# Kernel tuning notes

Measured on AMD Instinct MI355X. Metric: run time of the kernel, lower is better.

Reference implementation:

```python
import jax, jax.numpy as jnp
import numpy as np

H = 16  # num_heads

def _split_heads(x, h):
    B, T, D = x.shape
    return x.reshape(B, T, h, D // h).transpose(0, 2, 1, 3)  # [B,h,T,d]

def setup_inputs() -> dict:
    key = jax.random.key(0)
    ks = jax.random.split(key, 7)
    B, T, D = 2, 2048, 2048
    s = 0.02
    return {
        "x": jax.random.normal(ks[0], (B, T, D), dtype=jnp.float32),
        "Wq1": jax.random.normal(ks[1], (D, D), dtype=jnp.float32) * s,
        "Wq2": jax.random.normal(ks[2], (D, D), dtype=jnp.float32) * s,
        "Wk": jax.random.normal(ks[3], (D, D), dtype=jnp.float32) * s,
        "Wv": jax.random.normal(ks[4], (D, D), dtype=jnp.float32) * s,
        "Wlam": jax.random.normal(ks[5], (D, H), dtype=jnp.float32) * s,
        "Wo": jax.random.normal(ks[6], (D, D), dtype=jnp.float32) * s,
    }

def reference(x, Wq1, Wq2, Wk, Wv, Wlam, Wo):
    B, T, D = x.shape
    d = D // H
    q1 = _split_heads(x @ Wq1, H)
    q2 = _split_heads(x @ Wq2, H)
    k = _split_heads(x @ Wk, H)
    v = _split_heads(x @ Wv, H)
    q = jnp.concatenate([q1, q2], axis=1)        # [B,2H,T,d] (q1 heads then q2 heads)
    k2 = jnp.repeat(k, 2, axis=1)                # [B,2H,T,d] (adjacent duplication, as torch repeat_interleave)
    v2 = jnp.repeat(v, 2, axis=1)
    scale = 1.0 / jnp.sqrt(jnp.asarray(d, dtype=x.dtype))
    scores = jnp.einsum("bhqd,bhkd->bhqk", q, k2) * scale
    causal = jnp.tril(jnp.ones((T, T), dtype=bool))
    scores = jnp.where(causal, scores, jnp.finfo(scores.dtype).min)
    p = jax.nn.softmax(scores, axis=-1)
    y = jnp.einsum("bhqk,bhkd->bhqd", p, v2)     # [B,2H,T,d]
    y1, y2 = y[:, :H], y[:, H:]
    lam = jax.nn.sigmoid(x @ Wlam).transpose(0, 2, 1)[..., None]  # [B,H,T,1]
    y = y1 - lam * y2                            # [B,H,T,d]
    y = y.transpose(0, 2, 1, 3).reshape(B, T, D)
    return y @ Wo
```

## Files before the change

kernel.cpp:

```cpp
#include <hip/hip_runtime.h>
#include <stdint.h>

#define Bb 2
#define Tt 2048
#define Dd 2048
#define Hh 16
#define HD 128
#define NTOK (Bb*Tt)

typedef _Float16 f16;
typedef unsigned short u16;
typedef __attribute__((ext_vector_type(8))) _Float16 f16x8;
typedef __attribute__((ext_vector_type(4))) _Float16 f16x4;
typedef __attribute__((ext_vector_type(4))) float f32x4;

__device__ __forceinline__ void gl2lds16(const f16* g, f16* l) {
  __builtin_amdgcn_global_load_lds(
      (const __attribute__((address_space(1))) unsigned int*)(const_cast<f16*>(g)),
      (__attribute__((address_space(3))) unsigned int*)(l),
      16, 0, 0);
}

__global__ __launch_bounds__(256) void cvtlam_kernel(const float* __restrict__ x,
                                                     const float* __restrict__ Wlam,
                                                     f16* __restrict__ xh,
                                                     float* __restrict__ lamb) {
  const int wid = threadIdx.x >> 6, lane = threadIdx.x & 63;
  const int tok = blockIdx.x * 4 + wid;
  const float* xr = x + (size_t)tok * Dd;
  f16* xo = xh + (size_t)tok * Dd;
  float acc[16] = {};
#pragma unroll
  for (int j = 0; j < 8; ++j) {
    const int k0 = j * 256 + lane * 4;
    float4 v = *(const float4*)(xr + k0);
    f16x4 o;
    o.x = (f16)v.x; o.y = (f16)v.y; o.z = (f16)v.z; o.w = (f16)v.w;
    *(f16x4*)(xo + k0) = o;
    const float xe4[4] = {v.x, v.y, v.z, v.w};
#pragma unroll
    for (int e = 0; e < 4; ++e) {
      const float xe = xe4[e];
      const float4* wr = (const float4*)(Wlam + (size_t)(k0 + e) * Hh);
#pragma unroll
      for (int q = 0; q < 4; ++q) {
        float4 w = wr[q];
        acc[q * 4 + 0] = fmaf(xe, w.x, acc[q * 4 + 0]);
        acc[q * 4 + 1] = fmaf(xe, w.y, acc[q * 4 + 1]);
        acc[q * 4 + 2] = fmaf(xe, w.z, acc[q * 4 + 2]);
        acc[q * 4 + 3] = fmaf(xe, w.w, acc[q * 4 + 3]);
      }
    }
  }
#pragma unroll
  for (int ofs = 32; ofs >= 1; ofs >>= 1)
#pragma unroll
    for (int i = 0; i < 16; ++i) acc[i] += __shfl_xor(acc[i], ofs);
  if (lane == 0) {
#pragma unroll
    for (int i = 0; i < 16; ++i)
      lamb[tok * Hh + i] = 1.f / (1.f + __expf(-acc[i]));
  }
}

__global__ void wtrans_kernel(const float* __restrict__ W0, const float* __restrict__ W1,
                              const float* __restrict__ W2, const float* __restrict__ W3,
                              const float* __restrict__ W4, f16* __restrict__ wt) {
  const float* W;
  int z = blockIdx.z;
  if (z == 0) W = W0; else if (z == 1) W = W1; else if (z == 2) W = W2;
  else if (z == 3) W = W3; else W = W4;
  f16* dst = wt + (size_t)z * Dd * Dd;
  __shared__ f16 tile[64][65];
  const int k0 = blockIdx.y * 64, n0 = blockIdx.x * 64;
  const int tr = threadIdx.x >> 6, tc = threadIdx.x & 63;
#pragma unroll
  for (int p = 0; p < 16; ++p) {
    int r = tr + p * 4;
    tile[r][tc] = (f16)W[(size_t)(k0 + r) * Dd + n0 + tc];
  }
  __syncthreads();
#pragma unroll
  for (int p = 0; p < 16; ++p) {
    int r = tr + p * 4;
    dst[(size_t)(n0 + r) * Dd + k0 + tc] = tile[tc][r];
  }
}

template <int OUTF16>
__global__ __launch_bounds__(256) void gemm_bt_kernel(
    const f16* __restrict__ A, const f16* __restrict__ Bt0,
    unsigned long long bt_stride, void* __restrict__ Cb, unsigned long long c_stride) {
  __shared__ __align__(16) f16 Alds[128 * 32];
  __shared__ __align__(16) f16 Blds[128 * 32];
  const f16* Bt = Bt0 + (size_t)blockIdx.z * bt_stride;
  const int m0 = blockIdx.y * 128, n0 = blockIdx.x * 128;
  const int tid = threadIdx.x, wid = tid >> 6, lane = tid & 63;
  const int quad = lane >> 4, l15 = lane & 15;
  const int srow = lane >> 2, sch = lane & 3;
  const int g = (l15 >> 1) & 3;
  const int koff = (quad ^ g) * 8;
  const int mw = (wid >> 1) * 64, nw = (wid & 1) * 64;
  const int sg = sch ^ ((srow >> 1) & 3);
  f32x4 acc[4][4] = {};
  for (int kk = 0; kk < Dd; kk += 32) {
#pragma unroll
    for (int j = 0; j < 2; ++j) {
      const int c = wid * 2 + j;
      const int row = c * 16 + srow;
      gl2lds16(A + (size_t)(m0 + row) * Dd + kk + sg * 8, &Alds[c * 512]);
      gl2lds16(Bt + (size_t)(n0 + row) * Dd + kk + sg * 8, &Blds[c * 512]);
    }
    __syncthreads();
    f16x8 af[4], bfr[4];
#pragma unroll
    for (int t = 0; t < 4; ++t)
      af[t] = *(const f16x8*)&Alds[(mw + t * 16 + l15) * 32 + koff];
#pragma unroll
    for (int t = 0; t < 4; ++t)
      bfr[t] = *(const f16x8*)&Blds[(nw + t * 16 + l15) * 32 + koff];
#pragma unroll
    for (int mt = 0; mt < 4; ++mt)
#pragma unroll
      for (int nt = 0; nt < 4; ++nt)
        acc[mt][nt] = __builtin_amdgcn_mfma_f32_16x16x32_f16(af[mt], bfr[nt], acc[mt][nt], 0, 0, 0);
    __syncthreads();
  }
  const size_t czoff = (size_t)blockIdx.z * c_stride;
#pragma unroll
  for (int mt = 0; mt < 4; ++mt) {
    const int r0 = m0 + mw + mt * 16 + quad * 4;
#pragma unroll
    for (int r = 0; r < 4; ++r) {
#pragma unroll
      for (int nt = 0; nt < 4; ++nt) {
        const int col = n0 + nw + nt * 16 + l15;
        const float v = acc[mt][nt][r];
        if (OUTF16)
          ((f16*)Cb)[czoff + (size_t)(r0 + r) * Dd + col] = (f16)v;
        else
          ((float*)Cb)[czoff + (size_t)(r0 + r) * Dd + col] = v;
      }
    }
  }
}

__global__ void vtrans_kernel(const f16* __restrict__ vb, f16* __restrict__ vtb) {
  const int z = blockIdx.z;
  const int b = z >> 4, hv = z & 15;
  const int t0 = blockIdx.x * 64, d0 = blockIdx.y * 64;
  __shared__ f16 tile[64][65];
  const int tr = threadIdx.x >> 6, tc = threadIdx.x & 63;
#pragma unroll
  for (int p = 0; p < 16; ++p) {
    int r = tr + p * 4;
    tile[r][tc] = vb[(size_t)(b * Tt + t0 + r) * Dd + hv * HD + d0 + tc];
  }
  __syncthreads();
  const int u = tc & 31;
  const int tp = (tc & 32) | (((u >> 2) & 3) * 8 + ((u >> 4) & 1) * 4 + (u & 3));
#pragma unroll
  for (int p = 0; p < 16; ++p) {
    int r = tr + p * 4;
    vtb[((size_t)z * HD + d0 + r) * Tt + t0 + tp] = tile[tc][r];
  }
}

__global__ __launch_bounds__(256, 3) void attn_kernel(
    const f16* __restrict__ q1b, const f16* __restrict__ q2b,
    const f16* __restrict__ kbuf, const f16* __restrict__ vtb,
    f16* __restrict__ yah) {
  __shared__ __align__(16) f16 Klds[64 * 128];
  __shared__ __align__(16) f16 Vlds[2][128 * 64];
  const int bx = blockIdx.x;
  const int qt = (bx & 1) ? (15 - (bx >> 1)) : (bx >> 1);
  const int h = blockIdx.y, b = blockIdx.z;
  const int hkv = h >> 1;
  const f16* qb = (h < Hh) ? q1b : q2b;
  const int hq = h & 15;
  const int tid = threadIdx.x, wid = tid >> 6, lane = tid & 63;
  const int quad = lane >> 4, l15 = lane & 15;
  const int qbase = qt * 128 + wid * 32;
  const int ntiles = 2 * qt + 2;
  const f16 qscale = (f16)(0.08838834764831845f * 1.4426950408889634f);

  f16x8 qf0[4], qf1[4];
  {
    const f16* qp0 = qb + (size_t)(b * Tt + qbase + l15) * Dd + hq * HD + quad * 8;
    const f16* qp1 = qp0 + (size_t)16 * Dd;
#pragma unroll
    for (int ks = 0; ks < 4; ++ks) { qf0[ks] = *(const f16x8*)(qp0 + ks * 32); qf1[ks] = *(const f16x8*)(qp1 + ks * 32); }
#pragma unroll
    for (int ks = 0; ks < 4; ++ks) { qf0[ks] *= qscale; qf1[ks] *= qscale; }
  }

  uint32_t koffg[4], voffg[4];
#pragma unroll
  for (int p = 0; p < 4; ++p) {
    const int krow = wid * 16 + p * 4 + (lane >> 4);
    const int kch = (lane & 15) ^ (krow & 7);
    koffg[p] = (uint32_t)((b * Tt + krow) * Dd + hkv * HD + kch * 8);
    const int vrow = wid * 32 + p * 8 + (lane >> 3);
    const int vch = (lane & 7) ^ (vrow & 7);
    voffg[p] = (uint32_t)(((b * 16 + hkv) * HD + vrow) * Tt + vch * 8);
  }

  f32x4 o0[8] = {}, o1[8] = {};
  float m_0 = -3.0e38f, m_1 = -3.0e38f, l_0 = 0.f, l_1 = 0.f;

#define ISSUE_K(KT)                                                                \
  {                                                                                \
    const uint32_t kshift = (uint32_t)(KT) * 64 * Dd;                              \
    _Pragma("unroll") for (int p = 0; p < 4; ++p)                                  \
        gl2lds16(kbuf + kshift + koffg[p], &Klds[(wid * 16 + p * 4) * 128]);       \
  }
#define ISSUE_V(KT)                                                                \
  {                                                                                \
    const uint32_t vshift = (uint32_t)(KT) * 64;                                   \
    f16* vb_ = &Vlds[(KT) & 1][0];                                                 \
    _Pragma("unroll") for (int p = 0; p < 4; ++p)                                  \
        gl2lds16(vtb + vshift + voffg[p], &vb_[(wid * 32 + p * 8) * 64]);          \
  }

  ISSUE_K(0);
  ISSUE_V(0);

  for (int kt = 0; kt < ntiles; ++kt) {
    asm volatile("s_waitcnt vmcnt(4)\n\ts_barrier" ::: "memory");
    const bool live = (kt * 64 <= qbase + 31);
    f32x4 s0[4] = {}, s1[4] = {};
    if (live) {
#pragma unroll
      for (int nt = 0; nt < 4; ++nt) {
        const int r = nt * 16 + l15;
#pragma unroll
        for (int ks = 0; ks < 4; ++ks) {
          f16x8 kf = *(const f16x8*)&Klds[r * 128 + (((ks * 4 + quad) ^ (l15 & 7)) << 3)];
          s0[nt] = __builtin_amdgcn_mfma_f32_16x16x32_f16(kf, qf0[ks], s0[nt], 0, 0, 0);
          s1[nt] = __builtin_amdgcn_mfma_f32_16x16x32_f16(kf, qf1[ks], s1[nt], 0, 0, 0);
        }
      }
    }
    asm volatile("s_waitcnt vmcnt(0) lgkmcnt(0)\n\ts_barrier" ::: "memory");
    if (kt + 1 < ntiles) { ISSUE_K(kt + 1); ISSUE_V(kt + 1); }
    if (live) {
      const f16* Vl = &Vlds[kt & 1][0];
      if (kt * 64 + 63 > qbase) {
        const int q0 = qbase + l15, q1_ = q0 + 16;
#pragma unroll
        for (int nt = 0; nt < 4; ++nt) {
          const int keyb = kt * 64 + nt * 16 + quad * 4;
#pragma unroll
          for (int r = 0; r < 4; ++r) {
            if (keyb + r > q0) s0[nt][r] = -3.0e38f;
            if (keyb + r > q1_) s1[nt][r] = -3.0e38f;
          }
        }
      }
      float tm0 = s0[0][0], tm1 = s1[0][0];
#pragma unroll
      for (int nt = 0; nt < 4; ++nt)
#pragma unroll
        for (int r = 0; r < 4; ++r) { tm0 = fmaxf(tm0, s0[nt][r]); tm1 = fmaxf(tm1, s1[nt][r]); }
      tm0 = fmaxf(tm0, __shfl_xor(tm0, 16)); tm1 = fmaxf(tm1, __shfl_xor(tm1, 16));
      tm0 = fmaxf(tm0, __shfl_xor(tm0, 32)); tm1 = fmaxf(tm1, __shfl_xor(tm1, 32));
      const float mo0 = m_0, mo1 = m_1;
      m_0 = fmaxf(m_0, tm0); m_1 = fmaxf(m_1, tm1);
      float rs0 = 0.f, rs1 = 0.f;
      f16x4 pf0[4], pf1[4];
#pragma unroll
      for (int nt = 0; nt < 4; ++nt) {
        float a0 = exp2f(s0[nt][0] - m_0), a1 = exp2f(s0[nt][1] - m_0);
        float a2 = exp2f(s0[nt][2] - m_0), a3 = exp2f(s0[nt][3] - m_0);
        float b0 = exp2f(s1[nt][0] - m_1), b1 = exp2f(s1[nt][1] - m_1);
        float b2 = exp2f(s1[nt][2] - m_1), b3 = exp2f(s1[nt][3] - m_1);
        rs0 += (a0 + a1) + (a2 + a3);
        rs1 += (b0 + b1) + (b2 + b3);
        pf0[nt].x = (f16)a0; pf0[nt].y = (f16)a1; pf0[nt].z = (f16)a2; pf0[nt].w = (f16)a3;
        pf1[nt].x = (f16)b0; pf1[nt].y = (f16)b1; pf1[nt].z = (f16)b2; pf1[nt].w = (f16)b3;
      }
      rs0 += __shfl_xor(rs0, 16); rs1 += __shfl_xor(rs1, 16);
      rs0 += __shfl_xor(rs0, 32); rs1 += __shfl_xor(rs1, 32);
      if (__ballot((m_0 > mo0) | (m_1 > mo1))) {
        const float al0 = exp2f(mo0 - m_0), al1 = exp2f(mo1 - m_1);
        l_0 *= al0; l_1 *= al1;
        float ar0[4], ar1[4];
#pragma unroll
        for (int r = 0; r < 4; ++r) { ar0[r] = __shfl(al0, quad * 4 + r); ar1[r] = __shfl(al1, quad * 4 + r); }
#pragma unroll
        for (int n2 = 0; n2 < 8; ++n2)
#pragma unroll
          for (int r = 0; r < 4; ++r) { o0[n2][r] *= ar0[r]; o1[n2][r] *= ar1[r]; }
      }
      l_0 += rs0; l_1 += rs1;
#pragma unroll
      for (int g = 0; g < 2; ++g) {
#pragma unroll
        for (int n2 = 0; n2 < 8; ++n2) {
          const int d_ = n2 * 16 + l15;
          f16x8 vf = *(const f16x8*)&Vl[d_ * 64 + (((g * 4 + quad) ^ (l15 & 7)) << 3)];
          f16x4 vlo = __builtin_shufflevector(vf, vf, 0, 1, 2, 3);
          f16x4 vhi = __builtin_shufflevector(vf, vf, 4, 5, 6, 7);
          o0[n2] = __builtin_amdgcn_mfma_f32_16x16x16f16(pf0[2 * g], vlo, o0[n2], 0, 0, 0);
          o0[n2] = __builtin_amdgcn_mfma_f32_16x16x16f16(pf0[2 * g + 1], vhi, o0[n2], 0, 0, 0);
          o1[n2] = __builtin_amdgcn_mfma_f32_16x16x16f16(pf1[2 * g], vlo, o1[n2], 0, 0, 0);
          o1[n2] = __builtin_amdgcn_mfma_f32_16x16x16f16(pf1[2 * g + 1], vhi, o1[n2], 0, 0, 0);
        }
      }
    }
  }
#undef ISSUE_K
#undef ISSUE_V

  float lr0[4], lr1[4];
#pragma unroll
  for (int r = 0; r < 4; ++r) { lr0[r] = __shfl(l_0, quad * 4 + r); lr1[r] = __shfl(l_1, quad * 4 + r); }
#pragma unroll
  for (int r = 0; r < 4; ++r) {
    const float i0 = 1.0f / lr0[r], i1 = 1.0f / lr1[r];
    const int row0 = qbase + quad * 4 + r;
    f16* d0_ = yah + ((size_t)(b * 32 + h) * Tt + row0) * HD;
    f16* d1_ = d0_ + (size_t)16 * HD;
#pragma unroll
    for (int n2 = 0; n2 < 8; ++n2) {
      d0_[n2 * 16 + l15] = (f16)(o0[n2][r] * i0);
      d1_[n2 * 16 + l15] = (f16)(o1[n2][r] * i1);
    }
  }
}

__global__ void combine_kernel(const f16* __restrict__ yah, const float* __restrict__ lamb,
                               f16* __restrict__ ybf) {
  const int n4 = NTOK * Dd / 4;
  int i = blockIdx.x * 256 + threadIdx.x;
  const int stride = gridDim.x * 256;
  for (; i < n4; i += stride) {
    const int e0 = i * 4;
    const int dc = e0 & 127;
    const int hh = (e0 >> 7) & 15;
    const int tt = (e0 >> 11) & 2047;
    const int bb = e0 >> 22;
    const size_t base1 = ((size_t)(bb * 32 + hh) * Tt + tt) * HD + dc;
    const size_t base2 = ((size_t)(bb * 32 + 16 + hh) * Tt + tt) * HD + dc;
    f16x4 y1 = *(const f16x4*)(yah + base1);
    f16x4 y2 = *(const f16x4*)(yah + base2);
    const float lam = lamb[(bb * Tt + tt) * Hh + hh];
    f16x4 o;
    o.x = (f16)((float)y1.x - lam * (float)y2.x);
    o.y = (f16)((float)y1.y - lam * (float)y2.y);
    o.z = (f16)((float)y1.z - lam * (float)y2.z);
    o.w = (f16)((float)y1.w - lam * (float)y2.w);
    *(f16x4*)(ybf + e0) = o;
  }
}

extern "C" void kernel_launch(void* const* d_in, const int* in_sizes, int n_in,
                              void* d_out, int out_size, void* d_ws, size_t ws_size,
                              hipStream_t stream) {
  const float* x    = (const float*)d_in[0];
  const float* Wq1  = (const float*)d_in[1];
  const float* Wq2  = (const float*)d_in[2];
  const float* Wk   = (const float*)d_in[3];
  const float* Wv   = (const float*)d_in[4];
  const float* Wlam = (const float*)d_in[5];
  const float* Wo   = (const float*)d_in[6];

  f16* xbf = (f16*)d_ws;
  f16* wt  = xbf + (size_t)NTOK * Dd;
  f16* q1b = wt + 5ull * Dd * Dd;
  f16* q2b = q1b + (size_t)NTOK * Dd;
  f16* kbf = q2b + (size_t)NTOK * Dd;
  f16* vbf = kbf + (size_t)NTOK * Dd;
  f16* vtb = vbf + (size_t)NTOK * Dd;
  float* lamb = (float*)(vtb + (size_t)NTOK * Dd);
  f16* yah = (f16*)(lamb + (size_t)NTOK * Hh);
  f16* ybf = xbf;

  cvtlam_kernel<<<dim3(NTOK / 4), dim3(256), 0, stream>>>(x, Wlam, xbf, lamb);
  wtrans_kernel<<<dim3(32, 32, 5), dim3(256), 0, stream>>>(Wq1, Wq2, Wk, Wv, Wo, wt);
  gemm_bt_kernel<1><<<dim3(16, 32, 4), dim3(256), 0, stream>>>(
      xbf, wt, (unsigned long long)Dd * Dd, (void*)q1b, (unsigned long long)NTOK * Dd);
  vtrans_kernel<<<dim3(32, 2, 32), dim3(256), 0, stream>>>(vbf, vtb);
  attn_kernel<<<dim3(16, 32, 2), dim3(256), 0, stream>>>(q1b, q2b, kbf, vtb, yah);
  combine_kernel<<<dim3(2048), dim3(256), 0, stream>>>(yah, lamb, ybf);
  gemm_bt_kernel<0><<<dim3(16, 32, 1), dim3(256), 0, stream>>>(
      ybf, wt + 4ull * Dd * Dd, 0ull, d_out, 0ull);
}
```

Measured before the change: 774.9 us.

## Enlarge attention blocks to 8 waves with double-buffered K/V tiles

```diff
diff --git a/kernel.cpp b/kernel.cpp
--- a/kernel.cpp
+++ b/kernel.cpp
@@ -166,22 +166,22 @@
   }
 }
 
-__global__ __launch_bounds__(256, 3) void attn_kernel(
+__global__ __launch_bounds__(512, 4) void attn_kernel(
     const f16* __restrict__ q1b, const f16* __restrict__ q2b,
     const f16* __restrict__ kbuf, const f16* __restrict__ vtb,
     f16* __restrict__ yah) {
-  __shared__ __align__(16) f16 Klds[64 * 128];
+  __shared__ __align__(16) f16 Klds[2][64 * 128];
   __shared__ __align__(16) f16 Vlds[2][128 * 64];
   const int bx = blockIdx.x;
-  const int qt = (bx & 1) ? (15 - (bx >> 1)) : (bx >> 1);
+  const int qt = (bx & 1) ? (7 - (bx >> 1)) : (bx >> 1);
   const int h = blockIdx.y, b = blockIdx.z;
   const int hkv = h >> 1;
   const f16* qb = (h < Hh) ? q1b : q2b;
   const int hq = h & 15;
   const int tid = threadIdx.x, wid = tid >> 6, lane = tid & 63;
   const int quad = lane >> 4, l15 = lane & 15;
-  const int qbase = qt * 128 + wid * 32;
-  const int ntiles = 2 * qt + 2;
+  const int qbase = qt * 256 + wid * 32;
+  const int ntiles = 4 * qt + 4;
   const f16 qscale = (f16)(0.08838834764831845f * 1.4426950408889634f);
 
   f16x8 qf0[4], qf1[4];
@@ -194,57 +194,53 @@
     for (int ks = 0; ks < 4; ++ks) { qf0[ks] *= qscale; qf1[ks] *= qscale; }
   }
 
-  uint32_t koffg[4], voffg[4];
-#pragma unroll
-  for (int p = 0; p < 4; ++p) {
-    const int krow = wid * 16 + p * 4 + (lane >> 4);
+  uint32_t koffg[2], voffg[2];
+#pragma unroll
+  for (int c = 0; c < 2; ++c) {
+    const int krow = c * 32 + wid * 4 + (lane >> 4);
     const int kch = (lane & 15) ^ (krow & 7);
-    koffg[p] = (uint32_t)((b * Tt + krow) * Dd + hkv * HD + kch * 8);
-    const int vrow = wid * 32 + p * 8 + (lane >> 3);
+    koffg[c] = (uint32_t)((b * Tt + krow) * Dd + hkv * HD + kch * 8);
+    const int vrow = c * 64 + wid * 8 + (lane >> 3);
     const int vch = (lane & 7) ^ (vrow & 7);
-    voffg[p] = (uint32_t)(((b * 16 + hkv) * HD + vrow) * Tt + vch * 8);
+    voffg[c] = (uint32_t)(((b * 16 + hkv) * HD + vrow) * Tt + vch * 8);
   }
 
   f32x4 o0[8] = {}, o1[8] = {};
   float m_0 = -3.0e38f, m_1 = -3.0e38f, l_0 = 0.f, l_1 = 0.f;
 
-#define ISSUE_K(KT)                                                                \
-  {                                                                                \
-    const uint32_t kshift = (uint32_t)(KT) * 64 * Dd;                              \
-    _Pragma("unroll") for (int p = 0; p < 4; ++p)                                  \
-        gl2lds16(kbuf + kshift + koffg[p], &Klds[(wid * 16 + p * 4) * 128]);       \
-  }
-#define ISSUE_V(KT)                                                                \
-  {                                                                                \
-    const uint32_t vshift = (uint32_t)(KT) * 64;                                   \
-    f16* vb_ = &Vlds[(KT) & 1][0];                                                 \
-    _Pragma("unroll") for (int p = 0; p < 4; ++p)                                  \
-        gl2lds16(vtb + vshift + voffg[p], &vb_[(wid * 32 + p * 8) * 64]);          \
-  }
-
-  ISSUE_K(0);
-  ISSUE_V(0);
+#define ISSUE_TILE(KT, PAR)                                                          \
+  {                                                                                  \
+    const uint32_t kshift = (uint32_t)(KT) * 64 * Dd;                                \
+    const uint32_t vshift = (uint32_t)(KT) * 64;                                     \
+    _Pragma("unroll") for (int c = 0; c < 2; ++c)                                    \
+        gl2lds16(kbuf + kshift + koffg[c], &Klds[PAR][(c * 32 + wid * 4) * 128]);    \
+    _Pragma("unroll") for (int c = 0; c < 2; ++c)                                    \
+        gl2lds16(vtb + vshift + voffg[c], &Vlds[PAR][(c * 64 + wid * 8) * 64]);      \
+  }
+
+  ISSUE_TILE(0, 0);
+  ISSUE_TILE(1, 1);
 
   for (int kt = 0; kt < ntiles; ++kt) {
-    asm volatile("s_waitcnt vmcnt(4)\n\ts_barrier" ::: "memory");
-    const bool live = (kt * 64 <= qbase + 31);
-    f32x4 s0[4] = {}, s1[4] = {};
-    if (live) {
+    const int cur = kt & 1;
+    if (kt + 1 < ntiles) asm volatile("s_waitcnt vmcnt(4)\n\ts_barrier" ::: "memory");
+    else                 asm volatile("s_waitcnt vmcnt(0)\n\ts_barrier" ::: "memory");
+
+    if (kt * 64 <= qbase + 31) {
+      const f16* Kl = &Klds[cur][0];
+      const f16* Vl = &Vlds[cur][0];
+
+      f32x4 s0[4] = {}, s1[4] = {};
 #pragma unroll
       for (int nt = 0; nt < 4; ++nt) {
         const int r = nt * 16 + l15;
 #pragma unroll
         for (int ks = 0; ks < 4; ++ks) {
-          f16x8 kf = *(const f16x8*)&Klds[r * 128 + (((ks * 4 + quad) ^ (l15 & 7)) << 3)];
+          f16x8 kf = *(const f16x8*)&Kl[r * 128 + (((ks * 4 + quad) ^ (l15 & 7)) << 3)];
           s0[nt] = __builtin_amdgcn_mfma_f32_16x16x32_f16(kf, qf0[ks], s0[nt], 0, 0, 0);
           s1[nt] = __builtin_amdgcn_mfma_f32_16x16x32_f16(kf, qf1[ks], s1[nt], 0, 0, 0);
         }
       }
-    }
-    asm volatile("s_waitcnt vmcnt(0) lgkmcnt(0)\n\ts_barrier" ::: "memory");
-    if (kt + 1 < ntiles) { ISSUE_K(kt + 1); ISSUE_V(kt + 1); }
-    if (live) {
-      const f16* Vl = &Vlds[kt & 1][0];
       if (kt * 64 + 63 > qbase) {
         const int q0 = qbase + l15, q1_ = q0 + 16;
 #pragma unroll
@@ -295,22 +291,21 @@
       l_0 += rs0; l_1 += rs1;
 #pragma unroll
       for (int g = 0; g < 2; ++g) {
+        const f16x8 pf8_0 = __builtin_shufflevector(pf0[2 * g], pf0[2 * g + 1], 0, 1, 2, 3, 4, 5, 6, 7);
+        const f16x8 pf8_1 = __builtin_shufflevector(pf1[2 * g], pf1[2 * g + 1], 0, 1, 2, 3, 4, 5, 6, 7);
 #pragma unroll
         for (int n2 = 0; n2 < 8; ++n2) {
           const int d_ = n2 * 16 + l15;
           f16x8 vf = *(const f16x8*)&Vl[d_ * 64 + (((g * 4 + quad) ^ (l15 & 7)) << 3)];
-          f16x4 vlo = __builtin_shufflevector(vf, vf, 0, 1, 2, 3);
-          f16x4 vhi = __builtin_shufflevector(vf, vf, 4, 5, 6, 7);
-          o0[n2] = __builtin_amdgcn_mfma_f32_16x16x16f16(pf0[2 * g], vlo, o0[n2], 0, 0, 0);
-          o0[n2] = __builtin_amdgcn_mfma_f32_16x16x16f16(pf0[2 * g + 1], vhi, o0[n2], 0, 0, 0);
-          o1[n2] = __builtin_amdgcn_mfma_f32_16x16x16f16(pf1[2 * g], vlo, o1[n2], 0, 0, 0);
-          o1[n2] = __builtin_amdgcn_mfma_f32_16x16x16f16(pf1[2 * g + 1], vhi, o1[n2], 0, 0, 0);
+          o0[n2] = __builtin_amdgcn_mfma_f32_16x16x32_f16(pf8_0, vf, o0[n2], 0, 0, 0);
+          o1[n2] = __builtin_amdgcn_mfma_f32_16x16x32_f16(pf8_1, vf, o1[n2], 0, 0, 0);
         }
       }
     }
-  }
-#undef ISSUE_K
-#undef ISSUE_V
+    asm volatile("s_waitcnt lgkmcnt(0)\n\ts_barrier" ::: "memory");
+    if (kt + 2 < ntiles) ISSUE_TILE(kt + 2, cur);
+  }
+#undef ISSUE_TILE
 
   float lr0[4], lr1[4];
 #pragma unroll
@@ -381,7 +376,7 @@
   gemm_bt_kernel<1><<<dim3(16, 32, 4), dim3(256), 0, stream>>>(
       xbf, wt, (unsigned long long)Dd * Dd, (void*)q1b, (unsigned long long)NTOK * Dd);
   vtrans_kernel<<<dim3(32, 2, 32), dim3(256), 0, stream>>>(vbf, vtb);
-  attn_kernel<<<dim3(16, 32, 2), dim3(256), 0, stream>>>(q1b, q2b, kbf, vtb, yah);
+  attn_kernel<<<dim3(8, 32, 2), dim3(512), 0, stream>>>(q1b, q2b, kbf, vtb, yah);
   combine_kernel<<<dim3(2048), dim3(256), 0, stream>>>(yah, lamb, ybf);
   gemm_bt_kernel<0><<<dim3(16, 32, 1), dim3(256), 0, stream>>>(
       ybf, wt + 4ull * Dd * Dd, 0ull, d_out, 0ull);
```

Result: slower. 871.3 us (+12.4%).
